# Performance work log

Hardware: AMD Instinct MI355X
Metric: run time of the kernel (lower is better)

Reference implementation:

```python
import jax, jax.numpy as jnp
import numpy as np

B = 128
D = 128            # d_model
LENS = [512, 256, 128, 64]   # finest -> coarsest level lengths
ORDERS = [1, 2, 3, 4]        # front_block order, then front_blocks[0..2] orders


def freq_interp(x, target_len):
    # x: (B, C, L_in) -> (B, C, target_len). Zero-pad spectrum, scale by len ratio.
    l_in = x.shape[2]
    xf = jnp.fft.rfft(x, axis=2)                                  # (B,C,l_in//2+1)
    pad = target_len // 2 + 1 - xf.shape[2]
    of = jnp.pad(xf, ((0, 0), (0, 0), (0, pad)))
    out = jnp.fft.irfft(of, n=target_len, axis=2)
    return out * (l_in / target_len)


def cheby_kan(x, coeffs):
    # x: (B,N,C_in), coeffs: (C_in, C_out, deg+1). T_k(t) = cos(k*acos(t)).
    deg1 = coeffs.shape[2]
    theta = jnp.arccos(jnp.tanh(jnp.tanh(x)))                     # (B,N,C_in)
    basis = jnp.cos(theta[..., None] * jnp.arange(deg1, dtype=x.dtype))  # (B,N,C_in,deg+1)
    return jnp.einsum('bnid,iod->bno', basis, coeffs)


def dw_conv(x, w):
    # depthwise Conv1d, kernel 3, padding 1, no bias. x: (B,N,C), w: (C,3).
    xc = jnp.transpose(x, (0, 2, 1))                              # (B,C,N)
    k = w[:, None, :]                                             # (C,1,3) OIH
    y = jax.lax.conv_general_dilated(
        xc, k, window_strides=(1,), padding=[(1, 1)],
        dimension_numbers=('NCH', 'OIH', 'NCH'),
        feature_group_count=x.shape[2])
    return jnp.transpose(y, (0, 2, 1))


def m_kan(x, coeffs, w):
    return cheby_kan(x, coeffs) + dw_conv(x, w)


def setup_inputs():
    key = jax.random.key(0)
    ks = jax.random.split(key, 16)
    inp = {}
    for i, L in enumerate(LENS):
        inp[f'x{i}'] = jax.random.normal(ks[i], (B, L, D), dtype=jnp.float32)
    for j, order in enumerate(ORDERS):
        std = 1.0 / (D * (order + 1))
        inp[f'coeffs{j}'] = std * jax.random.normal(ks[4 + 2 * j], (D, D, order + 1), dtype=jnp.float32)
        inp[f'w{j}'] = 0.1 * jax.random.normal(ks[5 + 2 * j], (D, 3), dtype=jnp.float32)
    return inp


def reference(x0, x1, x2, x3,
              coeffs0, w0, coeffs1, w1, coeffs2, w2, coeffs3, w3):
    levels = [x0, x1, x2, x3]
    rev_lens = LENS[::-1]                      # [64, 128, 256, 512]

    # ---- FrequencyDecomp ----
    rev = levels[::-1]
    out_low, out_high = rev[0], rev[1]
    dec = [out_low]
    for i in range(len(rev) - 1):
        res = jnp.transpose(
            freq_interp(jnp.transpose(out_low, (0, 2, 1)), rev_lens[i + 1]), (0, 2, 1))
        dec.append(out_high - res)
        out_low = out_high
        if i + 2 <= len(rev) - 1:
            out_high = rev[i + 2]
    dec = dec[::-1]

    # ---- FrequencyMixing ----
    rev = dec[::-1]
    out_low = m_kan(rev[0], coeffs0, w0)       # front_block, order=begin_order
    out_high = rev[1]
    blocks = [(coeffs1, w1), (coeffs2, w2), (coeffs3, w3)]
    mix = [out_low]
    for i in range(len(rev) - 1):
        oh = m_kan(out_high, *blocks[i])
        res = jnp.transpose(
            freq_interp(jnp.transpose(out_low, (0, 2, 1)), rev_lens[i + 1]), (0, 2, 1))
        out_low = oh + res
        mix.append(out_low)
        if i + 2 <= len(rev) - 1:
            out_high = rev[i + 2]
    mix = mix[::-1]
    return tuple(mix)
```

## Files before the change

### kernel.cpp

```cpp
#include <hip/hip_runtime.h>
#include <math.h>

#define B_SZ 128
#define D_SZ 128

typedef __attribute__((ext_vector_type(8))) short bf16x8;
typedef __attribute__((ext_vector_type(4))) float f32x4;

__device__ __forceinline__ unsigned short f2bf(float f) {
    unsigned u = __float_as_uint(f);
    unsigned r = (u + 0x7FFF + ((u >> 16) & 1)) >> 16;
    return (unsigned short)r;
}

__device__ __forceinline__ void castT_tile(
    const float* __restrict__ src, unsigned short* __restrict__ dst,
    int b, int n0, int L)
{
    __shared__ unsigned short tt[128][72];
    const int tid = threadIdx.x;
    for (int i = tid; i < 64 * 32; i += 256) {
        int nr = i >> 5, c4 = (i & 31) * 4;
        float4 v = *(const float4*)(src + ((size_t)b * L + n0 + nr) * 128 + c4);
        tt[c4 + 0][nr] = f2bf(v.x);
        tt[c4 + 1][nr] = f2bf(v.y);
        tt[c4 + 2][nr] = f2bf(v.z);
        tt[c4 + 3][nr] = f2bf(v.w);
    }
    __syncthreads();
    const int c = tid >> 1, seg = (tid & 1) * 32;
    unsigned short* dp = dst + ((size_t)b * 128 + c) * L + n0 + seg;
    #pragma unroll
    for (int j = 0; j < 32; j += 8)
        *(bf16x8*)(dp + j) = *(const bf16x8*)&tt[c][seg + j];
}

__global__ __launch_bounds__(256) void prep_all(
    const float* __restrict__ x1, const float* __restrict__ x2,
    const float* __restrict__ x3,
    unsigned short* __restrict__ Xt1, unsigned short* __restrict__ Xt2,
    unsigned short* __restrict__ Xt3,
    unsigned short* __restrict__ U256, unsigned short* __restrict__ U128,
    unsigned short* __restrict__ U64p,
    const float* __restrict__ c0, const float* __restrict__ c1,
    const float* __restrict__ c2, const float* __restrict__ c3,
    unsigned short* __restrict__ BmT_all, float* __restrict__ bias_all)
{
    const int bid = blockIdx.x, tid = threadIdx.x;
    if (bid < 896) {
        if (bid < 512)      castT_tile(x1, Xt1, bid >> 2, (bid & 3) * 64, 256);
        else if (bid < 768) castT_tile(x2, Xt2, (bid - 512) >> 1, ((bid - 512) & 1) * 64, 128);
        else                castT_tile(x3, Xt3, bid - 768, 0, 64);
    } else if (bid < 1568) {
        int fid = (bid - 896) * 256 + tid;
        unsigned short* U; int L, lg, e;
        if (fid < 131072)      { U = U256; L = 256; lg = 8; e = fid; }
        else if (fid < 163840) { U = U128; L = 128; lg = 7; e = fid - 131072; }
        else                   { U = U64p; L = 64;  lg = 6; e = fid - 163840; }
        const int n = e & (L - 1);
        const int m = e >> lg;
        const int t = m >> 1;
        const float inv4L = 1.0f / (4.0f * (float)L);
        float val;
        if ((m & 1) == 0) {
            val = ((t == n) ? 0.25f : 0.0f) + (((t + n) & 1) ? -inv4L : inv4L);
        } else {
            int idx = (t - n) & (L - 1);
            double th = M_PI * (2.0 * idx + 1.0) / (2.0 * L);
            double ct = cos(th) / sin(th);
            val = (float)((idx & 1) ? -ct : ct) * inv4L;
        }
        U[e] = f2bf(val);
    } else {
        const int r   = bid - 1568;
        const int set = r >> 6;
        const int o   = ((r & 63) << 1) + (tid >> 7);
        const int i   = tid & 127;
        const int DEG1 = set + 2;
        const float* cc = (set == 0) ? c0 : (set == 1) ? c1 : (set == 2) ? c2 : c3;
        const float* cp = cc + ((size_t)i * 128 + o) * DEG1;
        unsigned short* Bm = BmT_all + (size_t)set * 65536;
        for (int d = 1; d < DEG1; ++d)
            Bm[(size_t)(d - 1) * 16384 + o * 128 + i] = f2bf(cp[d]);
        float s = cp[0];
        #pragma unroll
        for (int off = 32; off >= 1; off >>= 1) s += __shfl_down(s, off);
        __shared__ float red[4];
        if ((tid & 63) == 0) red[tid >> 6] = s;
        __syncthreads();
        if ((tid & 127) == 0)
            bias_all[set * 128 + o] = red[tid >> 6] + red[(tid >> 6) + 1];
    }
}

__device__ __forceinline__ void up2_body(
    const unsigned short* __restrict__ U,
    const unsigned short* __restrict__ Xt,
    const float* __restrict__ xh,
    float* __restrict__ out,
    unsigned short* __restrict__ xtm,
    float sign, int b, int mt, int L)
{
    const int NK = L >> 5;
    const int tid = threadIdx.x;
    __shared__ unsigned short Ab[2][2048];
    __shared__ unsigned short Bb[2][4096];

    const int ln = tid & 63, wv = tid >> 6;
    const int wm = wv & 1, wn = wv >> 1;
    const int lr = ln & 15, qd = ln >> 4;

    f32x4 acc[2][4];
    #pragma unroll
    for (int mi = 0; mi < 2; ++mi)
        #pragma unroll
        for (int nt = 0; nt < 4; ++nt)
            acc[mi][nt] = (f32x4){0.f, 0.f, 0.f, 0.f};

    const int arow = tid >> 2, acol = (tid & 3) * 8;

    auto stage = [&](int kk, int buf) {
        const unsigned short* ga = U + (size_t)(mt * 64 + arow) * L + kk * 32 + acol;
        ((bf16x8*)Ab[buf])[tid] = *(const bf16x8*)ga;
        #pragma unroll
        for (int j = 0; j < 2; ++j) {
            int sidx = tid + (j << 8);
            const unsigned short* gb =
                Xt + ((size_t)b * 128 + (sidx >> 2)) * L + kk * 32 + (sidx & 3) * 8;
            ((bf16x8*)Bb[buf])[sidx] = *(const bf16x8*)gb;
        }
    };

    stage(0, 0);
    for (int kk = 0; kk < NK; ++kk) {
        __syncthreads();
        if (kk + 1 < NK) stage(kk + 1, (kk + 1) & 1);
        const int buf = kk & 1;
        bf16x8 af[2], bfv[4];
        #pragma unroll
        for (int mi = 0; mi < 2; ++mi)
            af[mi] = *(const bf16x8*)&Ab[buf][(wm * 32 + mi * 16 + lr) * 32 + qd * 8];
        #pragma unroll
        for (int nt = 0; nt < 4; ++nt)
            bfv[nt] = *(const bf16x8*)&Bb[buf][(wn * 64 + nt * 16 + lr) * 32 + qd * 8];
        #pragma unroll
        for (int mi = 0; mi < 2; ++mi)
            #pragma unroll
            for (int nt = 0; nt < 4; ++nt)
                acc[mi][nt] = __builtin_amdgcn_mfma_f32_16x16x32_bf16(
                    af[mi], bfv[nt], acc[mi][nt], 0, 0, 0);
    }

    const int twoL = L << 1;
    #pragma unroll
    for (int nt = 0; nt < 4; ++nt) {
        const int col = wn * 64 + nt * 16 + lr;
        #pragma unroll
        for (int mi = 0; mi < 2; ++mi) {
            #pragma unroll
            for (int r = 0; r < 4; ++r) {
                const int row = mt * 64 + wm * 32 + mi * 16 + qd * 4 + r;
                const size_t gi = ((size_t)b * twoL + row) * 128 + col;
                float v = xh[gi] + sign * acc[mi][nt][r];
                out[gi] = v;
                if (xtm)
                    xtm[((size_t)b * 128 + col) * twoL + row] = f2bf(v);
            }
        }
    }
}

__global__ __launch_bounds__(256) void up2_dec(
    const unsigned short* __restrict__ U64p, const unsigned short* __restrict__ U128,
    const unsigned short* __restrict__ U256,
    const unsigned short* __restrict__ Xt3, const unsigned short* __restrict__ Xt2,
    const unsigned short* __restrict__ Xt1,
    const float* __restrict__ x2, const float* __restrict__ x1,
    const float* __restrict__ x0,
    float* __restrict__ d2, float* __restrict__ d1, float* __restrict__ d0)
{
    const int bid = blockIdx.x;
    const unsigned short *U, *Xt; const float* xh; float* out;
    int L, lgMT, base;
    if (bid < 256)      { U = U64p; Xt = Xt3; xh = x2; out = d2; L = 64;  lgMT = 1; base = 0; }
    else if (bid < 768) { U = U128; Xt = Xt2; xh = x1; out = d1; L = 128; lgMT = 2; base = 256; }
    else                { U = U256; Xt = Xt1; xh = x0; out = d0; L = 256; lgMT = 3; base = 768; }
    const int rb = bid - base;
    up2_body(U, Xt, xh, out, nullptr, -1.f, rb >> lgMT, rb & ((1 << lgMT) - 1), L);
}

__global__ __launch_bounds__(256) void up2_mix(
    const unsigned short* __restrict__ U, const unsigned short* __restrict__ Xt,
    float* __restrict__ m, unsigned short* __restrict__ xtm, int L, int lgMT)
{
    up2_body(U, Xt, m, m, xtm, 1.f,
             blockIdx.x >> lgMT, blockIdx.x & ((1 << lgMT) - 1), L);
}

__global__ __launch_bounds__(256) void mkan_all(
    const float* __restrict__ xa, const float* __restrict__ xb,
    const float* __restrict__ xc, const float* __restrict__ xd,
    const unsigned short* __restrict__ BmT_all,
    const float* __restrict__ bias_all,
    const float* __restrict__ w0p, const float* __restrict__ w1p,
    const float* __restrict__ w2p, const float* __restrict__ w3p,
    float* __restrict__ m0, float* __restrict__ m1,
    float* __restrict__ m2, float* __restrict__ m3,
    unsigned short* __restrict__ xtm0)
{
    __shared__ unsigned short As[16384];
    __shared__ unsigned short Bb[2][4096];

    const int bid = blockIdx.x, tid = threadIdx.x;
    const float *x, *w; float* outp; unsigned short* xtm = nullptr;
    int set, mb, Lmask;
    if (bid < 256)       { x = xa; w = w0p; outp = m0; set = 0; mb = bid << 5;          Lmask = 63;  xtm = xtm0; }
    else if (bid < 768)  { x = xb; w = w1p; outp = m1; set = 1; mb = (bid - 256) << 5;  Lmask = 127; }
    else if (bid < 1792) { x = xc; w = w2p; outp = m2; set = 2; mb = (bid - 768) << 5;  Lmask = 255; }
    else                 { x = xd; w = w3p; outp = m3; set = 3; mb = (bid - 1792) << 5; Lmask = 511; }
    const int deg1m1 = set + 1;
    const int NK = deg1m1 << 2;
    const unsigned short* Bm = BmT_all + (size_t)set * 65536;
    const float* bias = bias_all + (set << 7);

    for (int e = tid * 4; e < 4096; e += 1024) {
        const int row = e >> 7, i = e & 127;
        float4 v = *(const float4*)(x + ((size_t)(mb + row)) * 128 + i);
        float u0 = tanhf(tanhf(v.x)), u1 = tanhf(tanhf(v.y));
        float u2 = tanhf(tanhf(v.z)), u3 = tanhf(tanhf(v.w));
        float tp0 = 1.f, tp1 = 1.f, tp2 = 1.f, tp3 = 1.f;
        float tc0 = u0, tc1 = u1, tc2 = u2, tc3 = u3;
        unsigned short* ap0 = &As[((i >> 5) << 10) + (row << 5) + (i & 31)];
        for (int p = 0; p < deg1m1; ++p) {
            unsigned short* ap = ap0 + (p << 12);
            ap[0] = f2bf(tc0); ap[1] = f2bf(tc1);
            ap[2] = f2bf(tc2); ap[3] = f2bf(tc3);
            float tn0 = fmaf(2.f * u0, tc0, -tp0); tp0 = tc0; tc0 = tn0;
            float tn1 = fmaf(2.f * u1, tc1, -tp1); tp1 = tc1; tc1 = tn1;
            float tn2 = fmaf(2.f * u2, tc2, -tp2); tp2 = tc2; tc2 = tn2;
            float tn3 = fmaf(2.f * u3, tc3, -tp3); tp3 = tc3; tc3 = tn3;
        }
    }

    const int ln = tid & 63, wv = tid >> 6;
    const int wm = wv & 1, wn = wv >> 1;
    const int lr = ln & 15, qd = ln >> 4;

    f32x4 acc[4];
    #pragma unroll
    for (int nt = 0; nt < 4; ++nt) acc[nt] = (f32x4){0.f, 0.f, 0.f, 0.f};

    auto stageB = [&](int kk, int buf) {
        const int p = kk >> 2, i0 = (kk & 3) << 5;
        #pragma unroll
        for (int j = 0; j < 2; ++j) {
            int sidx = tid + (j << 8);
            const unsigned short* gb =
                Bm + (size_t)((p << 7) + (sidx >> 2)) * 128 + i0 + ((sidx & 3) << 3);
            ((bf16x8*)Bb[buf])[sidx] = *(const bf16x8*)gb;
        }
    };

    stageB(0, 0);
    for (int kk = 0; kk < NK; ++kk) {
        __syncthreads();
        if (kk + 1 < NK) stageB(kk + 1, (kk + 1) & 1);
        const int buf = kk & 1;
        bf16x8 af = *(const bf16x8*)&As[(kk << 10) + (((wm << 4) + lr) << 5) + (qd << 3)];
        bf16x8 bfv[4];
        #pragma unroll
        for (int nt = 0; nt < 4; ++nt)
            bfv[nt] = *(const bf16x8*)&Bb[buf][(((wn << 6) + (nt << 4) + lr) << 5) + (qd << 3)];
        #pragma unroll
        for (int nt = 0; nt < 4; ++nt)
            acc[nt] = __builtin_amdgcn_mfma_f32_16x16x32_bf16(af, bfv[nt], acc[nt], 0, 0, 0);
    }

    #pragma unroll
    for (int nt = 0; nt < 4; ++nt) {
        const int col = (wn << 6) + (nt << 4) + lr;
        const float ww0 = w[col * 3 + 0], ww1 = w[col * 3 + 1], ww2 = w[col * 3 + 2];
        const float bs = bias[col];
        #pragma unroll
        for (int r = 0; r < 4; ++r) {
            const int row = (wm << 4) + (qd << 2) + r;
            const int gm = mb + row;
            const int n = gm & Lmask;
            const size_t gi = (size_t)gm * 128 + col;
            float xm1 = (n > 0)     ? x[gi - 128] : 0.f;
            float x0v = x[gi];
            float xp1 = (n < Lmask) ? x[gi + 128] : 0.f;
            float v = acc[nt][r] + bs + fmaf(ww0, xm1, fmaf(ww1, x0v, ww2 * xp1));
            outp[gi] = v;
            if (xtm)
                xtm[(size_t)(((gm >> 6) << 7) + col) * 64 + (gm & 63)] = f2bf(v);
        }
    }
}

extern "C" void kernel_launch(void* const* d_in, const int* in_sizes, int n_in,
                              void* d_out, int out_size, void* d_ws, size_t ws_size,
                              hipStream_t stream) {
    const float* x0 = (const float*)d_in[0];
    const float* x1 = (const float*)d_in[1];
    const float* x2 = (const float*)d_in[2];
    const float* x3 = (const float*)d_in[3];
    const float* c0 = (const float*)d_in[4];
    const float* w0 = (const float*)d_in[5];
    const float* c1 = (const float*)d_in[6];
    const float* w1 = (const float*)d_in[7];
    const float* c2 = (const float*)d_in[8];
    const float* w2 = (const float*)d_in[9];
    const float* c3 = (const float*)d_in[10];
    const float* w3 = (const float*)d_in[11];
    float* out = (float*)d_out;

    float* d0 = (float*)d_ws;
    float* d1 = d0 + 8388608;
    float* d2 = d1 + 4194304;
    unsigned short* Xt1  = (unsigned short*)(d2 + 2097152);
    unsigned short* Xt2  = Xt1 + 4194304;
    unsigned short* Xt3  = Xt2 + 2097152;
    unsigned short* Xtm0 = Xt3 + 1048576;
    unsigned short* Xtm1 = Xtm0 + 1048576;
    unsigned short* Xtm2 = Xtm1 + 2097152;
    unsigned short* BmT  = Xtm2 + 4194304;
    float* bias_all = (float*)(BmT + 262144);
    unsigned short* U256 = (unsigned short*)(bias_all + 512);
    unsigned short* U128 = U256 + 131072;
    unsigned short* U64p = U128 + 32768;

    float* m3 = out;
    float* m2 = m3 + 8388608;
    float* m1 = m2 + 4194304;
    float* m0 = m1 + 2097152;

    prep_all<<<1824, 256, 0, stream>>>(x1, x2, x3, Xt1, Xt2, Xt3,
                                       U256, U128, U64p,
                                       c0, c1, c2, c3, BmT, bias_all);

    up2_dec<<<1792, 256, 0, stream>>>(U64p, U128, U256, Xt3, Xt2, Xt1,
                                      x2, x1, x0, d2, d1, d0);

    mkan_all<<<3840, 256, 0, stream>>>(x3, d2, d1, d0, BmT, bias_all,
                                       w0, w1, w2, w3, m0, m1, m2, m3, Xtm0);

    up2_mix<<<256,  256, 0, stream>>>(U64p, Xtm0, m1, Xtm1, 64, 1);
    up2_mix<<<512,  256, 0, stream>>>(U128, Xtm1, m2, Xtm2, 128, 2);
    up2_mix<<<1024, 256, 0, stream>>>(U256, Xtm2, m3, nullptr, 256, 3);
}
```

Baseline: 288.0 us.

## Load MFMA operands directly from global into registers and use fast tanh

Removes LDS staging and per-iteration __syncthreads from the upsample GEMM and the KAN GEMM B operand. Each lane now loads its own MFMA fragments straight from global memory, with a register-level one-step prefetch. Also replaces tanhf with an exp2/rcp based approximation. This trades shared-memory reuse and coalescing for fewer barriers and LDS traffic, and adds small accuracy loss in tanh.

```diff
diff --git a/kernel.cpp b/kernel.cpp
--- a/kernel.cpp
+++ b/kernel.cpp
@@ -11,6 +11,11 @@
     unsigned u = __float_as_uint(f);
     unsigned r = (u + 0x7FFF + ((u >> 16) & 1)) >> 16;
     return (unsigned short)r;
+}
+
+__device__ __forceinline__ float fast_tanh(float x) {
+    float e2 = __builtin_amdgcn_exp2f(x * 2.885390081777927f);
+    return fmaf(-2.0f, __builtin_amdgcn_rcpf(e2 + 1.0f), 1.0f);
 }
 
 __device__ __forceinline__ void castT_tile(
@@ -103,9 +108,6 @@
 {
     const int NK = L >> 5;
     const int tid = threadIdx.x;
-    __shared__ unsigned short Ab[2][2048];
-    __shared__ unsigned short Bb[2][4096];
-
     const int ln = tid & 63, wv = tid >> 6;
     const int wm = wv & 1, wn = wv >> 1;
     const int lr = ln & 15, qd = ln >> 4;
@@ -117,38 +119,40 @@
         for (int nt = 0; nt < 4; ++nt)
             acc[mi][nt] = (f32x4){0.f, 0.f, 0.f, 0.f};
 
-    const int arow = tid >> 2, acol = (tid & 3) * 8;
-
-    auto stage = [&](int kk, int buf) {
-        const unsigned short* ga = U + (size_t)(mt * 64 + arow) * L + kk * 32 + acol;
-        ((bf16x8*)Ab[buf])[tid] = *(const bf16x8*)ga;
-        #pragma unroll
-        for (int j = 0; j < 2; ++j) {
-            int sidx = tid + (j << 8);
-            const unsigned short* gb =
-                Xt + ((size_t)b * 128 + (sidx >> 2)) * L + kk * 32 + (sidx & 3) * 8;
-            ((bf16x8*)Bb[buf])[sidx] = *(const bf16x8*)gb;
-        }
-    };
-
-    stage(0, 0);
+    const unsigned short* Ap = U + (size_t)(mt * 64 + wm * 32 + lr) * L + (qd << 3);
+    const unsigned short* Bp = Xt + ((size_t)b * 128 + (wn << 6) + lr) * L + (qd << 3);
+    const int aStride = L << 4;
+    const int bStride = L << 4;
+
+    bf16x8 ac[2], bc[4], an[2], bn[4];
+    #pragma unroll
+    for (int mi = 0; mi < 2; ++mi) ac[mi] = *(const bf16x8*)(Ap + mi * aStride);
+    #pragma unroll
+    for (int nt = 0; nt < 4; ++nt) bc[nt] = *(const bf16x8*)(Bp + nt * bStride);
+
     for (int kk = 0; kk < NK; ++kk) {
-        __syncthreads();
-        if (kk + 1 < NK) stage(kk + 1, (kk + 1) & 1);
-        const int buf = kk & 1;
-        bf16x8 af[2], bfv[4];
-        #pragma unroll
-        for (int mi = 0; mi < 2; ++mi)
-            af[mi] = *(const bf16x8*)&Ab[buf][(wm * 32 + mi * 16 + lr) * 32 + qd * 8];
-        #pragma unroll
-        for (int nt = 0; nt < 4; ++nt)
-            bfv[nt] = *(const bf16x8*)&Bb[buf][(wn * 64 + nt * 16 + lr) * 32 + qd * 8];
+        const bool pf = (kk + 1 < NK);
+        if (pf) {
+            const int ko = (kk + 1) << 5;
+            #pragma unroll
+            for (int mi = 0; mi < 2; ++mi)
+                an[mi] = *(const bf16x8*)(Ap + mi * aStride + ko);
+            #pragma unroll
+            for (int nt = 0; nt < 4; ++nt)
+                bn[nt] = *(const bf16x8*)(Bp + nt * bStride + ko);
+        }
         #pragma unroll
         for (int mi = 0; mi < 2; ++mi)
             #pragma unroll
             for (int nt = 0; nt < 4; ++nt)
                 acc[mi][nt] = __builtin_amdgcn_mfma_f32_16x16x32_bf16(
-                    af[mi], bfv[nt], acc[mi][nt], 0, 0, 0);
+                    ac[mi], bc[nt], acc[mi][nt], 0, 0, 0);
+        if (pf) {
+            #pragma unroll
+            for (int mi = 0; mi < 2; ++mi) ac[mi] = an[mi];
+            #pragma unroll
+            for (int nt = 0; nt < 4; ++nt) bc[nt] = bn[nt];
+        }
     }
 
     const int twoL = L << 1;
@@ -209,7 +213,6 @@
     unsigned short* __restrict__ xtm0)
 {
     __shared__ unsigned short As[16384];
-    __shared__ unsigned short Bb[2][4096];
 
     const int bid = blockIdx.x, tid = threadIdx.x;
     const float *x, *w; float* outp; unsigned short* xtm = nullptr;
@@ -226,8 +229,8 @@
     for (int e = tid * 4; e < 4096; e += 1024) {
         const int row = e >> 7, i = e & 127;
         float4 v = *(const float4*)(x + ((size_t)(mb + row)) * 128 + i);
-        float u0 = tanhf(tanhf(v.x)), u1 = tanhf(tanhf(v.y));
-        float u2 = tanhf(tanhf(v.z)), u3 = tanhf(tanhf(v.w));
+        float u0 = fast_tanh(fast_tanh(v.x)), u1 = fast_tanh(fast_tanh(v.y));
+        float u2 = fast_tanh(fast_tanh(v.z)), u3 = fast_tanh(fast_tanh(v.w));
         float tp0 = 1.f, tp1 = 1.f, tp2 = 1.f, tp3 = 1.f;
         float tc0 = u0, tc1 = u1, tc2 = u2, tc3 = u3;
         unsigned short* ap0 = &As[((i >> 5) << 10) + (row << 5) + (i & 31)];
@@ -250,30 +253,32 @@
     #pragma unroll
     for (int nt = 0; nt < 4; ++nt) acc[nt] = (f32x4){0.f, 0.f, 0.f, 0.f};
 
-    auto stageB = [&](int kk, int buf) {
-        const int p = kk >> 2, i0 = (kk & 3) << 5;
-        #pragma unroll
-        for (int j = 0; j < 2; ++j) {
-            int sidx = tid + (j << 8);
-            const unsigned short* gb =
-                Bm + (size_t)((p << 7) + (sidx >> 2)) * 128 + i0 + ((sidx & 3) << 3);
-            ((bf16x8*)Bb[buf])[sidx] = *(const bf16x8*)gb;
-        }
-    };
-
-    stageB(0, 0);
+    const unsigned short* Bp = Bm + (((wn << 6) + lr) << 7) + (qd << 3);
+    const unsigned short* Asp = &As[(((wm << 4) + lr) << 5) + (qd << 3)];
+
+    bf16x8 bc[4], bn[4];
+    #pragma unroll
+    for (int nt = 0; nt < 4; ++nt)
+        bc[nt] = *(const bf16x8*)(Bp + (nt << 11));
+
+    __syncthreads();
+
     for (int kk = 0; kk < NK; ++kk) {
-        __syncthreads();
-        if (kk + 1 < NK) stageB(kk + 1, (kk + 1) & 1);
-        const int buf = kk & 1;
-        bf16x8 af = *(const bf16x8*)&As[(kk << 10) + (((wm << 4) + lr) << 5) + (qd << 3)];
-        bf16x8 bfv[4];
+        const bool pf = (kk + 1 < NK);
+        if (pf) {
+            const int off = (((kk + 1) >> 2) << 14) + (((kk + 1) & 3) << 5);
+            #pragma unroll
+            for (int nt = 0; nt < 4; ++nt)
+                bn[nt] = *(const bf16x8*)(Bp + (nt << 11) + off);
+        }
+        bf16x8 af = *(const bf16x8*)(Asp + (kk << 10));
         #pragma unroll
         for (int nt = 0; nt < 4; ++nt)
-            bfv[nt] = *(const bf16x8*)&Bb[buf][(((wn << 6) + (nt << 4) + lr) << 5) + (qd << 3)];
-        #pragma unroll
-        for (int nt = 0; nt < 4; ++nt)
-            acc[nt] = __builtin_amdgcn_mfma_f32_16x16x32_bf16(af, bfv[nt], acc[nt], 0, 0, 0);
+            acc[nt] = __builtin_amdgcn_mfma_f32_16x16x32_bf16(af, bc[nt], acc[nt], 0, 0, 0);
+        if (pf) {
+            #pragma unroll
+            for (int nt = 0; nt < 4; ++nt) bc[nt] = bn[nt];
+        }
     }
 
     #pragma unroll
```

New measurement: 345.4 us. 1.2x slower.
